# Performance work log

Hardware: AMD Instinct MI355X
Metric: run time of the kernel (lower is better)

Reference implementation:

```python
import jax, jax.numpy as jnp
import numpy as np

N = 5
CASCADING_LOSS = 0.85
MAX_VAL = 255.0


def _warp(img, flow):
    """Bilinear warp of img [C,H,W] by flow [H,W,2], matching
    F.grid_sample(align_corners=True, padding_mode='zeros') where the
    sampling grid is pixel coords (w + flow_x, h + flow_y)."""
    C, H, W = img.shape
    px = jnp.arange(W, dtype=img.dtype)[None, :] + flow[..., 0]  # [H,W]
    py = jnp.arange(H, dtype=img.dtype)[:, None] + flow[..., 1]  # [H,W]
    x0 = jnp.floor(px)
    y0 = jnp.floor(py)
    wx1 = px - x0
    wy1 = py - y0
    wx0 = 1.0 - wx1
    wy0 = 1.0 - wy1

    def gather(xi, yi):
        valid = (xi >= 0) & (xi <= W - 1) & (yi >= 0) & (yi <= H - 1)
        xc = jnp.clip(xi, 0, W - 1).astype(jnp.int32)
        yc = jnp.clip(yi, 0, H - 1).astype(jnp.int32)
        v = img[:, yc, xc]  # [C,H,W]
        return v * valid[None, :, :].astype(img.dtype)

    out = (gather(x0, y0) * (wx0 * wy0)[None]
           + gather(x0 + 1, y0) * (wx1 * wy0)[None]
           + gather(x0, y0 + 1) * (wx0 * wy1)[None]
           + gather(x0 + 1, y0 + 1) * (wx1 * wy1)[None])
    return out  # [C,H,W]


def _psnr(ref, est):
    mse = jnp.mean((ref - est) ** 2)
    return 10.0 * jnp.log10(MAX_VAL * MAX_VAL / mse)


def setup_inputs() -> dict:
    key = jax.random.key(0)
    k1, k2, k3 = jax.random.split(key, 3)
    H, W = 1080, 1920
    flow_tup = jax.random.normal(k1, (N, H, W, 2), dtype=jnp.float32) * 5.0
    frame1 = jax.random.uniform(k2, (3, H, W), dtype=jnp.float32) * 255.0
    frame2 = jax.random.uniform(k3, (3, H, W), dtype=jnp.float32) * 255.0
    return {"flow_tup": flow_tup, "frame1": frame1, "frame2": frame2}


def reference(flow_tup, frame1, frame2):
    # warp frame1 by each of the N flows (vectorized over the cascade)
    warped = jax.vmap(lambda f: _warp(frame1, f))(flow_tup)  # [N,C,H,W]
    # torch .to(torch.uint8): truncate toward zero (values stay in [0,255])
    estim = jnp.trunc(warped)
    psnrs = jax.vmap(lambda e: _psnr(frame2, e))(estim)  # [N]
    weights = CASCADING_LOSS ** (N - jnp.arange(N, dtype=jnp.float32))
    aggr = jnp.sum(psnrs * weights)
    return -aggr
```

## Files before the change

kernel.cpp:

```cpp
#include <hip/hip_runtime.h>
#include <math.h>

#define IMG_H 1080
#define IMG_W 1920
#define NFLOW 5
#define HW (IMG_H * IMG_W)

#define TILE_W 64
#define TILE_H 32
#define HALO 32
#define REG_W (TILE_W + 2 * HALO)
#define REG_H (TILE_H + 2 * HALO)
#define THREADS 256
#define PX_PER_BLOCK (TILE_W * TILE_H)

__global__ __launch_bounds__(256) void pack_u8_kernel(const float* __restrict__ f1,
                                                      unsigned int* __restrict__ img)
{
    const int p = blockIdx.x * 256 + threadIdx.x;
    if (p >= HW) return;
    const unsigned r = (unsigned)(int)(f1[p] + 0.5f);
    const unsigned g = (unsigned)(int)(f1[HW + p] + 0.5f);
    const unsigned b = (unsigned)(int)(f1[2 * HW + p] + 0.5f);
    img[p] = r | (g << 8) | (b << 16);
}

__global__ __launch_bounds__(THREADS) void psnr_tile_kernel(
    const float2* __restrict__ flow,
    const unsigned int* __restrict__ img,
    const float* __restrict__ f2,
    float* __restrict__ sums)
{
    __shared__ unsigned int tile[REG_H * REG_W];
    __shared__ float sacc[NFLOW][4];

    const int tx0 = blockIdx.x * TILE_W;
    const int ty0 = blockIdx.y * TILE_H;
    const int tid = threadIdx.x;
    const int bx = tx0 - HALO;
    const int by = ty0 - HALO;

    for (int r = tid; r < REG_H * REG_W; r += THREADS) {
        const int ry = r >> 7;
        const int rx = r & (REG_W - 1);
        const int gx = bx + rx;
        const int gy = by + ry;
        if ((unsigned)gx < (unsigned)IMG_W && (unsigned)gy < (unsigned)IMG_H)
            tile[r] = img[gy * IMG_W + gx];
    }
    __syncthreads();

    const int sx0 = (bx > 0) ? bx : 0;
    const int sy0 = (by > 0) ? by : 0;
    const int sx1i = tx0 + TILE_W - 1 + HALO;
    const int sy1i = ty0 + TILE_H - 1 + HALO;
    const int sx1 = (sx1i < IMG_W - 1) ? sx1i : (IMG_W - 1);
    const int sy1 = (sy1i < IMG_H - 1) ? sy1i : (IMG_H - 1);
    const float sx0f = (float)sx0, sx1f = (float)sx1;
    const float sy0f = (float)sy0, sy1f = (float)sy1;

    float acc[NFLOW];
#pragma unroll
    for (int n = 0; n < NFLOW; ++n) acc[n] = 0.0f;

#pragma unroll
    for (int it = 0; it < PX_PER_BLOCK / THREADS; ++it) {
        const int q = it * THREADS + tid;
        const int ly = q >> 6;
        const int lx = q & 63;
        const int gx = tx0 + lx;
        const int gy = ty0 + ly;
        if (gy >= IMG_H) continue;
        const int p = gy * IMG_W + gx;

        const float r0 = f2[p];
        const float r1 = f2[HW + p];
        const float r2 = f2[2 * HW + p];

#pragma unroll
        for (int n = 0; n < NFLOW; ++n) {
            const float2 fl = flow[n * HW + p];
            const float px = (float)gx + fl.x;
            const float py = (float)gy + fl.y;
            const float x0f = floorf(px);
            const float y0f = floorf(py);
            const float wx1 = px - x0f;
            const float wy1 = py - y0f;
            const float wx0 = 1.0f - wx1;
            const float wy0 = 1.0f - wy1;
            const float x1f = x0f + 1.0f;
            const float y1f = y0f + 1.0f;

            const bool vx0 = (x0f >= 0.0f) && (x0f <= (float)(IMG_W - 1));
            const bool vx1 = (x1f >= 0.0f) && (x1f <= (float)(IMG_W - 1));
            const bool vy0 = (y0f >= 0.0f) && (y0f <= (float)(IMG_H - 1));
            const bool vy1 = (y1f >= 0.0f) && (y1f <= (float)(IMG_H - 1));

            const float w00 = (vx0 && vy0) ? (wx0 * wy0) : 0.0f;
            const float w10 = (vx1 && vy0) ? (wx1 * wy0) : 0.0f;
            const float w01 = (vx0 && vy1) ? (wx0 * wy1) : 0.0f;
            const float w11 = (vx1 && vy1) ? (wx1 * wy1) : 0.0f;

            const int x0i = (int)x0f;
            const int y0i = (int)y0f;
            const int x1i = x0i + 1;
            const int y1i = y0i + 1;

            const bool bad =
                ((x0f >= 0.0f) && (x0i < sx0)) ||
                ((x1f <= (float)(IMG_W - 1)) && (x1i > sx1)) ||
                ((y0f >= 0.0f) && (y0i < sy0)) ||
                ((y1f <= (float)(IMG_H - 1)) && (y1i > sy1));

            unsigned v00, v10, v01, v11;
            if (!bad) {
                const int rx0 = ((x0i > sx0) ? ((x0i < sx1) ? x0i : sx1) : sx0) - bx;
                const int rx1 = ((x1i > sx0) ? ((x1i < sx1) ? x1i : sx1) : sx0) - bx;
                const int ry0 = ((y0i > sy0) ? ((y0i < sy1) ? y0i : sy1) : sy0) - by;
                const int ry1 = ((y1i > sy0) ? ((y1i < sy1) ? y1i : sy1) : sy0) - by;
                v00 = tile[ry0 * REG_W + rx0];
                v10 = tile[ry0 * REG_W + rx1];
                v01 = tile[ry1 * REG_W + rx0];
                v11 = tile[ry1 * REG_W + rx1];
            } else {
                const int cx0 = (x0i > 0) ? ((x0i < IMG_W - 1) ? x0i : IMG_W - 1) : 0;
                const int cx1 = (x1i > 0) ? ((x1i < IMG_W - 1) ? x1i : IMG_W - 1) : 0;
                const int cy0 = (y0i > 0) ? ((y0i < IMG_H - 1) ? y0i : IMG_H - 1) : 0;
                const int cy1 = (y1i > 0) ? ((y1i < IMG_H - 1) ? y1i : IMG_H - 1) : 0;
                v00 = img[cy0 * IMG_W + cx0];
                v10 = img[cy0 * IMG_W + cx1];
                v01 = img[cy1 * IMG_W + cx0];
                v11 = img[cy1 * IMG_W + cx1];
            }

            const float e0 = (float)(v00 & 255u) * w00 + (float)(v10 & 255u) * w10 +
                             (float)(v01 & 255u) * w01 + (float)(v11 & 255u) * w11;
            const float e1 = (float)((v00 >> 8) & 255u) * w00 + (float)((v10 >> 8) & 255u) * w10 +
                             (float)((v01 >> 8) & 255u) * w01 + (float)((v11 >> 8) & 255u) * w11;
            const float e2 = (float)((v00 >> 16) & 255u) * w00 + (float)((v10 >> 16) & 255u) * w10 +
                             (float)((v01 >> 16) & 255u) * w01 + (float)((v11 >> 16) & 255u) * w11;

            const float d0 = r0 - truncf(e0);
            const float d1 = r1 - truncf(e1);
            const float d2 = r2 - truncf(e2);
            acc[n] += d0 * d0 + d1 * d1 + d2 * d2;
        }
    }

#pragma unroll
    for (int n = 0; n < NFLOW; ++n) {
#pragma unroll
        for (int off = 32; off > 0; off >>= 1)
            acc[n] += __shfl_down(acc[n], off, 64);
    }
    const int lane = threadIdx.x & 63;
    const int wid = threadIdx.x >> 6;
    if (lane == 0) {
#pragma unroll
        for (int n = 0; n < NFLOW; ++n) sacc[n][wid] = acc[n];
    }
    __syncthreads();
    if (threadIdx.x == 0) {
#pragma unroll
        for (int n = 0; n < NFLOW; ++n)
            atomicAdd(&sums[n], sacc[n][0] + sacc[n][1] + sacc[n][2] + sacc[n][3]);
    }
}

__global__ void psnr_finalize_kernel(const float* __restrict__ sums,
                                     float* __restrict__ out)
{
    if (threadIdx.x == 0 && blockIdx.x == 0) {
        double aggr = 0.0;
        for (int n = 0; n < NFLOW; ++n) {
            const double mse = (double)sums[n] / (3.0 * (double)HW);
            const double psnr = 10.0 * log10(255.0 * 255.0 / mse);
            double wgt = 1.0;
            for (int k = 0; k < NFLOW - n; ++k) wgt *= 0.85;
            aggr += psnr * wgt;
        }
        out[0] = (float)(-aggr);
    }
}

extern "C" void kernel_launch(void* const* d_in, const int* in_sizes, int n_in,
                              void* d_out, int out_size, void* d_ws, size_t ws_size,
                              hipStream_t stream) {
    const float* flow = (const float*)d_in[0];
    const float* f1   = (const float*)d_in[1];
    const float* f2   = (const float*)d_in[2];
    float* out = (float*)d_out;

    float* sums = (float*)d_ws;
    unsigned int* img = (unsigned int*)((char*)d_ws + 256);

    hipMemsetAsync(sums, 0, NFLOW * sizeof(float), stream);

    const int pack_blocks = (HW + 255) / 256;
    pack_u8_kernel<<<pack_blocks, 256, 0, stream>>>(f1, img);

    dim3 grid(IMG_W / TILE_W, (IMG_H + TILE_H - 1) / TILE_H);
    psnr_tile_kernel<<<grid, THREADS, 0, stream>>>((const float2*)flow, img, f2, sums);

    psnr_finalize_kernel<<<1, 64, 0, stream>>>(sums, out);
}
```

Baseline: 279.1 us.

## Fuse pack, warp-PSNR and finalize into one kernel with XCD-aware tile mapping

Removes the separate u8 pack kernel by quantizing frame1 into the shared-memory halo tile while loading it, and folds the finalize step into the main kernel using a last-block atomic counter. The halo shrinks from 32 to 24, which cuts shared memory per block and allows more blocks per CU. A per-flow bounds test on the flow value selects either a direct tile lookup or a global float fallback. Block IDs are remapped so neighbouring tiles land on the same XCD for L2 locality. In exchange, every block rounds three halo-padded float channels instead of reading one packed word per pixel, and the fallback path reads unrounded float pixels, which could differ from the rounded u8 values used on the tile path.

```diff
diff --git a/kernel.cpp b/kernel.cpp
--- a/kernel.cpp
+++ b/kernel.cpp
@@ -8,66 +8,66 @@
 
 #define TILE_W 64
 #define TILE_H 32
-#define HALO 32
+#define HALO 24
 #define REG_W (TILE_W + 2 * HALO)
 #define REG_H (TILE_H + 2 * HALO)
 #define THREADS 256
-#define PX_PER_BLOCK (TILE_W * TILE_H)
+#define GRID_X (IMG_W / TILE_W)
+#define GRID_Y ((IMG_H + TILE_H - 1) / TILE_H)
+#define NBLOCKS (GRID_X * GRID_Y)
 
-__global__ __launch_bounds__(256) void pack_u8_kernel(const float* __restrict__ f1,
-                                                      unsigned int* __restrict__ img)
-{
-    const int p = blockIdx.x * 256 + threadIdx.x;
-    if (p >= HW) return;
-    const unsigned r = (unsigned)(int)(f1[p] + 0.5f);
-    const unsigned g = (unsigned)(int)(f1[HW + p] + 0.5f);
-    const unsigned b = (unsigned)(int)(f1[2 * HW + p] + 0.5f);
-    img[p] = r | (g << 8) | (b << 16);
-}
-
-__global__ __launch_bounds__(THREADS) void psnr_tile_kernel(
+__global__ __launch_bounds__(THREADS, 4) void psnr_mega_kernel(
     const float2* __restrict__ flow,
-    const unsigned int* __restrict__ img,
+    const float* __restrict__ f1,
     const float* __restrict__ f2,
-    float* __restrict__ sums)
+    float* __restrict__ sums,
+    unsigned int* __restrict__ counter,
+    float* __restrict__ out)
 {
     __shared__ unsigned int tile[REG_H * REG_W];
     __shared__ float sacc[NFLOW][4];
 
-    const int tx0 = blockIdx.x * TILE_W;
-    const int ty0 = blockIdx.y * TILE_H;
-    const int tid = threadIdx.x;
+    const int wg = blockIdx.x;
+    const int xcd = wg & 7;
+    const int idx = wg >> 3;
+    const int q = NBLOCKS >> 3;
+    const int rr = NBLOCKS & 7;
+    const int wgid = (xcd < rr ? xcd * (q + 1) : rr * (q + 1) + (xcd - rr) * q) + idx;
+    const int tyb = wgid / GRID_X;
+    const int txb = wgid - tyb * GRID_X;
+
+    const int tx0 = txb * TILE_W;
+    const int ty0 = tyb * TILE_H;
     const int bx = tx0 - HALO;
     const int by = ty0 - HALO;
+    const int tid = threadIdx.x;
 
     for (int r = tid; r < REG_H * REG_W; r += THREADS) {
-        const int ry = r >> 7;
-        const int rx = r & (REG_W - 1);
+        const int ry = r / REG_W;
+        const int rx = r - ry * REG_W;
         const int gx = bx + rx;
         const int gy = by + ry;
-        if ((unsigned)gx < (unsigned)IMG_W && (unsigned)gy < (unsigned)IMG_H)
-            tile[r] = img[gy * IMG_W + gx];
+        unsigned v = 0u;
+        if ((unsigned)gx < (unsigned)IMG_W && (unsigned)gy < (unsigned)IMG_H) {
+            const int gp = gy * IMG_W + gx;
+            const unsigned c0 = (unsigned)(int)(f1[gp] + 0.5f);
+            const unsigned c1 = (unsigned)(int)(f1[HW + gp] + 0.5f);
+            const unsigned c2 = (unsigned)(int)(f1[2 * HW + gp] + 0.5f);
+            v = c0 | (c1 << 8) | (c2 << 16);
+        }
+        tile[r] = v;
     }
     __syncthreads();
-
-    const int sx0 = (bx > 0) ? bx : 0;
-    const int sy0 = (by > 0) ? by : 0;
-    const int sx1i = tx0 + TILE_W - 1 + HALO;
-    const int sy1i = ty0 + TILE_H - 1 + HALO;
-    const int sx1 = (sx1i < IMG_W - 1) ? sx1i : (IMG_W - 1);
-    const int sy1 = (sy1i < IMG_H - 1) ? sy1i : (IMG_H - 1);
-    const float sx0f = (float)sx0, sx1f = (float)sx1;
-    const float sy0f = (float)sy0, sy1f = (float)sy1;
 
     float acc[NFLOW];
 #pragma unroll
     for (int n = 0; n < NFLOW; ++n) acc[n] = 0.0f;
 
-#pragma unroll
-    for (int it = 0; it < PX_PER_BLOCK / THREADS; ++it) {
-        const int q = it * THREADS + tid;
-        const int ly = q >> 6;
-        const int lx = q & 63;
+#pragma unroll 4
+    for (int it = 0; it < (TILE_W * TILE_H) / THREADS; ++it) {
+        const int qq = it * THREADS + tid;
+        const int ly = qq >> 6;
+        const int lx = qq & 63;
         const int gx = tx0 + lx;
         const int gy = ty0 + ly;
         if (gy >= IMG_H) continue;
@@ -80,6 +80,9 @@
 #pragma unroll
         for (int n = 0; n < NFLOW; ++n) {
             const float2 fl = flow[n * HW + p];
+            const bool ok = (fl.x >= -(float)HALO) && (fl.x < (float)HALO) &&
+                            (fl.y >= -(float)HALO) && (fl.y < (float)HALO);
+
             const float px = (float)gx + fl.x;
             const float py = (float)gy + fl.y;
             const float x0f = floorf(px);
@@ -88,57 +91,48 @@
             const float wy1 = py - y0f;
             const float wx0 = 1.0f - wx1;
             const float wy0 = 1.0f - wy1;
-            const float x1f = x0f + 1.0f;
-            const float y1f = y0f + 1.0f;
 
             const bool vx0 = (x0f >= 0.0f) && (x0f <= (float)(IMG_W - 1));
-            const bool vx1 = (x1f >= 0.0f) && (x1f <= (float)(IMG_W - 1));
+            const bool vx1 = (x0f >= -1.0f) && (x0f <= (float)(IMG_W - 2));
             const bool vy0 = (y0f >= 0.0f) && (y0f <= (float)(IMG_H - 1));
-            const bool vy1 = (y1f >= 0.0f) && (y1f <= (float)(IMG_H - 1));
+            const bool vy1 = (y0f >= -1.0f) && (y0f <= (float)(IMG_H - 2));
 
             const float w00 = (vx0 && vy0) ? (wx0 * wy0) : 0.0f;
             const float w10 = (vx1 && vy0) ? (wx1 * wy0) : 0.0f;
             const float w01 = (vx0 && vy1) ? (wx0 * wy1) : 0.0f;
             const float w11 = (vx1 && vy1) ? (wx1 * wy1) : 0.0f;
 
-            const int x0i = (int)x0f;
-            const int y0i = (int)y0f;
-            const int x1i = x0i + 1;
-            const int y1i = y0i + 1;
+            float e0, e1, e2;
+            if (ok) {
+                const int x0i = (int)x0f;
+                const int y0i = (int)y0f;
+                const int ri = (y0i - by) * REG_W + (x0i - bx);
+                const unsigned v00 = tile[ri];
+                const unsigned v10 = tile[ri + 1];
+                const unsigned v01 = tile[ri + REG_W];
+                const unsigned v11 = tile[ri + REG_W + 1];
 
-            const bool bad =
-                ((x0f >= 0.0f) && (x0i < sx0)) ||
-                ((x1f <= (float)(IMG_W - 1)) && (x1i > sx1)) ||
-                ((y0f >= 0.0f) && (y0i < sy0)) ||
-                ((y1f <= (float)(IMG_H - 1)) && (y1i > sy1));
-
-            unsigned v00, v10, v01, v11;
-            if (!bad) {
-                const int rx0 = ((x0i > sx0) ? ((x0i < sx1) ? x0i : sx1) : sx0) - bx;
-                const int rx1 = ((x1i > sx0) ? ((x1i < sx1) ? x1i : sx1) : sx0) - bx;
-                const int ry0 = ((y0i > sy0) ? ((y0i < sy1) ? y0i : sy1) : sy0) - by;
-                const int ry1 = ((y1i > sy0) ? ((y1i < sy1) ? y1i : sy1) : sy0) - by;
-                v00 = tile[ry0 * REG_W + rx0];
-                v10 = tile[ry0 * REG_W + rx1];
-                v01 = tile[ry1 * REG_W + rx0];
-                v11 = tile[ry1 * REG_W + rx1];
+                e0 = (float)(v00 & 255u) * w00 + (float)(v10 & 255u) * w10 +
+                     (float)(v01 & 255u) * w01 + (float)(v11 & 255u) * w11;
+                e1 = (float)((v00 >> 8) & 255u) * w00 + (float)((v10 >> 8) & 255u) * w10 +
+                     (float)((v01 >> 8) & 255u) * w01 + (float)((v11 >> 8) & 255u) * w11;
+                e2 = (float)((v00 >> 16) & 255u) * w00 + (float)((v10 >> 16) & 255u) * w10 +
+                     (float)((v01 >> 16) & 255u) * w01 + (float)((v11 >> 16) & 255u) * w11;
             } else {
-                const int cx0 = (x0i > 0) ? ((x0i < IMG_W - 1) ? x0i : IMG_W - 1) : 0;
-                const int cx1 = (x1i > 0) ? ((x1i < IMG_W - 1) ? x1i : IMG_W - 1) : 0;
-                const int cy0 = (y0i > 0) ? ((y0i < IMG_H - 1) ? y0i : IMG_H - 1) : 0;
-                const int cy1 = (y1i > 0) ? ((y1i < IMG_H - 1) ? y1i : IMG_H - 1) : 0;
-                v00 = img[cy0 * IMG_W + cx0];
-                v10 = img[cy0 * IMG_W + cx1];
-                v01 = img[cy1 * IMG_W + cx0];
-                v11 = img[cy1 * IMG_W + cx1];
+                const int x0i = (int)fminf(fmaxf(x0f, 0.0f), (float)(IMG_W - 1));
+                const int x1i = (int)fminf(fmaxf(x0f + 1.0f, 0.0f), (float)(IMG_W - 1));
+                const int y0i = (int)fminf(fmaxf(y0f, 0.0f), (float)(IMG_H - 1));
+                const int y1i = (int)fminf(fmaxf(y0f + 1.0f, 0.0f), (float)(IMG_H - 1));
+                const int i00 = y0i * IMG_W + x0i;
+                const int i10 = y0i * IMG_W + x1i;
+                const int i01 = y1i * IMG_W + x0i;
+                const int i11 = y1i * IMG_W + x1i;
+                e0 = f1[i00] * w00 + f1[i10] * w10 + f1[i01] * w01 + f1[i11] * w11;
+                e1 = f1[HW + i00] * w00 + f1[HW + i10] * w10 +
+                     f1[HW + i01] * w01 + f1[HW + i11] * w11;
+                e2 = f1[2 * HW + i00] * w00 + f1[2 * HW + i10] * w10 +
+                     f1[2 * HW + i01] * w01 + f1[2 * HW + i11] * w11;
             }
-
-            const float e0 = (float)(v00 & 255u) * w00 + (float)(v10 & 255u) * w10 +
-                             (float)(v01 & 255u) * w01 + (float)(v11 & 255u) * w11;
-            const float e1 = (float)((v00 >> 8) & 255u) * w00 + (float)((v10 >> 8) & 255u) * w10 +
-                             (float)((v01 >> 8) & 255u) * w01 + (float)((v11 >> 8) & 255u) * w11;
-            const float e2 = (float)((v00 >> 16) & 255u) * w00 + (float)((v10 >> 16) & 255u) * w10 +
-                             (float)((v01 >> 16) & 255u) * w01 + (float)((v11 >> 16) & 255u) * w11;
 
             const float d0 = r0 - truncf(e0);
             const float d1 = r1 - truncf(e1);
@@ -160,26 +154,27 @@
         for (int n = 0; n < NFLOW; ++n) sacc[n][wid] = acc[n];
     }
     __syncthreads();
-    if (threadIdx.x == 0) {
+
+    if (tid == 0) {
 #pragma unroll
         for (int n = 0; n < NFLOW; ++n)
             atomicAdd(&sums[n], sacc[n][0] + sacc[n][1] + sacc[n][2] + sacc[n][3]);
-    }
-}
 
-__global__ void psnr_finalize_kernel(const float* __restrict__ sums,
-                                     float* __restrict__ out)
-{
-    if (threadIdx.x == 0 && blockIdx.x == 0) {
-        double aggr = 0.0;
-        for (int n = 0; n < NFLOW; ++n) {
-            const double mse = (double)sums[n] / (3.0 * (double)HW);
-            const double psnr = 10.0 * log10(255.0 * 255.0 / mse);
-            double wgt = 1.0;
-            for (int k = 0; k < NFLOW - n; ++k) wgt *= 0.85;
-            aggr += psnr * wgt;
+        __threadfence();
+        if (atomicAdd(counter, 1u) == (unsigned)(NBLOCKS - 1)) {
+            __threadfence();
+            double aggr = 0.0;
+            for (int n = 0; n < NFLOW; ++n) {
+                const float sn = __hip_atomic_load(&sums[n], __ATOMIC_RELAXED,
+                                                   __HIP_MEMORY_SCOPE_AGENT);
+                const double mse = (double)sn / (3.0 * (double)HW);
+                const double psnr = 10.0 * log10(255.0 * 255.0 / mse);
+                double wgt = 1.0;
+                for (int k = 0; k < NFLOW - n; ++k) wgt *= 0.85;
+                aggr += psnr * wgt;
+            }
+            out[0] = (float)(-aggr);
         }
-        out[0] = (float)(-aggr);
     }
 }
 
@@ -192,15 +187,9 @@
     float* out = (float*)d_out;
 
     float* sums = (float*)d_ws;
-    unsigned int* img = (unsigned int*)((char*)d_ws + 256);
+    unsigned int* counter = (unsigned int*)((char*)d_ws + 32);
 
-    hipMemsetAsync(sums, 0, NFLOW * sizeof(float), stream);
-
-    const int pack_blocks = (HW + 255) / 256;
-    pack_u8_kernel<<<pack_blocks, 256, 0, stream>>>(f1, img);
-
-    dim3 grid(IMG_W / TILE_W, (IMG_H + TILE_H - 1) / TILE_H);
-    psnr_tile_kernel<<<grid, THREADS, 0, stream>>>((const float2*)flow, img, f2, sums);
-
-    psnr_finalize_kernel<<<1, 64, 0, stream>>>(sums, out);
+    hipMemsetAsync(d_ws, 0, 64, stream);
+    psnr_mega_kernel<<<NBLOCKS, THREADS, 0, stream>>>(
+        (const float2*)flow, f1, f2, sums, counter, out);
 }
```

After: 253.1 us. 1.1x faster.
